# Optimization experiments

Hardware: AMD Instinct MI355X
Metric: run time of the kernel (lower is better)

## Reference

```python
import jax, jax.numpy as jnp
import numpy as np


def setup_inputs() -> dict:
    key = jax.random.key(0)
    k0, k1, k2, k3 = jax.random.split(key, 4)
    B, N, D, C, F = 8192, 784, 64, 10, 2  # batch, input_dim, bond_dim, num_classes, feature_dim
    x = jax.random.uniform(k0, (B, N), dtype=jnp.float32)  # pixel values in [0,1]
    core0 = jax.random.normal(k1, (F, 1, D), dtype=jnp.float32) * 0.1
    base = jnp.broadcast_to(jnp.eye(D, dtype=jnp.float32), (N - 2, F, D, D))
    cores_mid = base + jax.random.normal(k2, (N - 2, F, D, D), dtype=jnp.float32) * 0.01
    core_last = jax.random.normal(k3, (F, D, C), dtype=jnp.float32) * 0.1
    return {"x": x, "core0": core0, "cores_mid": cores_mid, "core_last": core_last}


def reference(x, core0, cores_mid, core_last):
    EPS = 1e-8
    factor = jnp.float32(np.pi / 2.0)
    # FeatureMap: [B, N] -> [B, N, 2] with (cos, sin)
    feats = jnp.stack([jnp.cos(factor * x), jnp.sin(factor * x)], axis=-1)
    # First site: M = v0 @ A0.squeeze(1)  -> [B, D]
    M = jnp.einsum('bf,fd->bd', feats[:, 0, :], core0[:, 0, :])
    # Sequential left->right contraction over middle sites with per-step L2 normalization
    v_mid = jnp.moveaxis(feats[:, 1:-1, :], 1, 0)  # [N-2, B, 2]

    def step(M, inp):
        v, A = inp  # v: [B, 2], A: [2, D, D]
        Mn = jnp.einsum('bi,bf,fij->bj', M, v, A)
        Mn = Mn / (jnp.linalg.norm(Mn, axis=1, keepdims=True) + EPS)
        return Mn, None

    M, _ = jax.lax.scan(step, M, (v_mid, cores_mid))
    # Last site: logits[b,c] = sum_i M[b,i] * (v_N[b,f] A_N[f,i,c])
    logits = jnp.einsum('bi,bf,fic->bc', M, feats[:, -1, :], core_last)
    return logits
```

## Files before the change

kernel.cpp:

```cpp
#include <hip/hip_runtime.h>

typedef __attribute__((ext_vector_type(8))) short s16x8;
typedef __attribute__((ext_vector_type(4))) float f32x4;
typedef __attribute__((ext_vector_type(4))) int i32x4;

#define NMID 782
#define PI_2 1.5707963267948966f
#define EG_STEP_BYTES 16384
#define EG_ELEMS ((size_t)NMID * 8192)
#define SLAB_B 2304
#define DBUF_B 4608

__device__ __forceinline__ int cvt_pk_bf16(float a, float b) {
  int r;
  asm("v_cvt_pk_bf16_f32 %0, %1, %2" : "=v"(r) : "v"(a), "v"(b));
  return r;
}

__device__ __forceinline__ f32x4 mfma_bf16(i32x4 a, i32x4 b, f32x4 c) {
  return __builtin_amdgcn_mfma_f32_16x16x32_bf16(
      __builtin_bit_cast(s16x8, a), __builtin_bit_cast(s16x8, b), c, 0, 0, 0);
}

__device__ __forceinline__ unsigned short bf16_rne(float v) {
  unsigned u = __float_as_uint(v);
  return (unsigned short)((u + 0x7FFFu + ((u >> 16) & 1)) >> 16);
}

__global__ __launch_bounds__(256) void prep_eg(const float* __restrict__ cm,
                                               unsigned short* __restrict__ eg) {
  const int n = blockIdx.x;
  const float* src = cm + (size_t)n * 8192;
  unsigned short* dst = eg + (size_t)n * 8192;
#pragma unroll
  for (int it = 0; it < 4; ++it) {
    int row = it * 256 + threadIdx.x;
    int q = row >> 6, l = row & 63;
    int t = q >> 2, cc = q & 3;
    int f = cc >> 1, c2 = cc & 1, h = l >> 4;
    int j = 16 * t + (l & 15);
    unsigned short v8[8];
#pragma unroll
    for (int e = 0; e < 8; ++e) {
      int i = 32 * c2 + 16 * (e >> 2) + 4 * h + (e & 3);
      float val = src[(f * 64 + i) * 64 + j] - (i == j ? 1.0f : 0.0f);
      v8[e] = bf16_rne(val);
    }
    *(uint4*)(dst + (size_t)row * 8) = *(const uint4*)v8;
  }
}

#define STEP2G(nc, CUR, NXT, C0, S0, C1, S1)                                \
  {                                                                         \
    int np = (nc) + 3;                                                      \
    if (np >= NMID) np = NMID - 1;                                          \
    const char* pnxt = base + (size_t)np * EG_STEP_BYTES;                   \
    _Pragma("unroll") for (int q = 0; q < 4; ++q)                           \
        NXT[q] = *(const i32x4*)(pnxt + q * 1024);                          \
    f32x4 z = {0.f, 0.f, 0.f, 0.f};                                         \
    __builtin_amdgcn_s_setprio(1);                                          \
    f32x4 aA0 = mfma_bf16(CUR[0], B0g0, z);                                 \
    aA0 = mfma_bf16(CUR[1], B1g0, aA0);                                     \
    f32x4 aB0 = mfma_bf16(CUR[2], B0g0, z);                                 \
    aB0 = mfma_bf16(CUR[3], B1g0, aB0);                                     \
    f32x4 aA1 = mfma_bf16(CUR[0], B0g1, z);                                 \
    aA1 = mfma_bf16(CUR[1], B1g1, aA1);                                     \
    f32x4 aB1 = mfma_bf16(CUR[2], B0g1, z);                                 \
    aB1 = mfma_bf16(CUR[3], B1g1, aB1);                                     \
    __builtin_amdgcn_s_setprio(0);                                          \
    char* wb = xlds + (((nc) + 1) & 1) * DBUF_B + bl * 144 + h * 32 +       \
               wv * 8;                                                      \
    float cps0 = (C0) + (S0);                                               \
    f32x4 mn0;                                                              \
    _Pragma("unroll") for (int r = 0; r < 4; ++r)                           \
        mn0[r] = cps0 * own0[r] + (C0)*aA0[r] + (S0)*aB0[r];                \
    own0 = mn0;                                                             \
    int2 w0;                                                                \
    w0.x = cvt_pk_bf16(mn0[0], mn0[1]);                                     \
    w0.y = cvt_pk_bf16(mn0[2], mn0[3]);                                     \
    *(int2*)(wb) = w0;                                                      \
    float cps1 = (C1) + (S1);                                               \
    f32x4 mn1;                                                              \
    _Pragma("unroll") for (int r = 0; r < 4; ++r)                           \
        mn1[r] = cps1 * own1[r] + (C1)*aA1[r] + (S1)*aB1[r];                \
    own1 = mn1;                                                             \
    int2 w1;                                                                \
    w1.x = cvt_pk_bf16(mn1[0], mn1[1]);                                     \
    w1.y = cvt_pk_bf16(mn1[2], mn1[3]);                                     \
    *(int2*)(wb + SLAB_B) = w1;                                             \
    asm volatile("s_waitcnt lgkmcnt(0)" ::: "memory");                      \
    __builtin_amdgcn_s_barrier();                                           \
    __builtin_amdgcn_sched_barrier(0);                                      \
    {                                                                       \
      const char* rb =                                                      \
          xlds + (((nc) + 1) & 1) * DBUF_B + bl * 144 + h * 32;             \
      B0g0 = *(const i32x4*)(rb);                                           \
      B1g0 = *(const i32x4*)(rb + 16);                                      \
      B0g1 = *(const i32x4*)(rb + SLAB_B);                                  \
      B1g1 = *(const i32x4*)(rb + SLAB_B + 16);                             \
    }                                                                       \
  }

__global__ __launch_bounds__(256, 1) void mps_main(
    const float* __restrict__ x, const float* __restrict__ core0,
    const float* __restrict__ core_last, const unsigned short* __restrict__ eg,
    float* __restrict__ out) {
  __shared__ alignas(16) char xlds[2 * DBUF_B];
  const int lane = threadIdx.x & 63;
  const int wv = threadIdx.x >> 6;
  const int bl = lane & 15;
  const int h = lane >> 4;
  const int b0 = blockIdx.x * 32 + bl;
  const int b1 = b0 + 16;
  const float* xr0 = x + (size_t)b0 * 784;
  const float* xr1 = x + (size_t)b1 * 784;
  const char* base = (const char*)eg + (size_t)wv * 4096 + (size_t)lane * 16;

  f32x4 own0, own1;
  i32x4 B0g0, B1g0, B0g1, B1g1;
  {
    float s, c;
    __sincosf(PI_2 * xr0[0], &s, &c);
    float fm[16];
#pragma unroll
    for (int t = 0; t < 4; ++t)
#pragma unroll
      for (int r = 0; r < 4; ++r) {
        int j = 16 * t + 4 * h + r;
        fm[t * 4 + r] = c * core0[j] + s * core0[64 + j];
      }
#pragma unroll
    for (int r = 0; r < 4; ++r) own0[r] = fm[wv * 4 + r];
#pragma unroll
    for (int p = 0; p < 4; ++p) {
      B0g0[p] = cvt_pk_bf16(fm[2 * p], fm[2 * p + 1]);
      B1g0[p] = cvt_pk_bf16(fm[8 + 2 * p], fm[8 + 2 * p + 1]);
    }
  }
  {
    float s, c;
    __sincosf(PI_2 * xr1[0], &s, &c);
    float fm[16];
#pragma unroll
    for (int t = 0; t < 4; ++t)
#pragma unroll
      for (int r = 0; r < 4; ++r) {
        int j = 16 * t + 4 * h + r;
        fm[t * 4 + r] = c * core0[j] + s * core0[64 + j];
      }
#pragma unroll
    for (int r = 0; r < 4; ++r) own1[r] = fm[wv * 4 + r];
#pragma unroll
    for (int p = 0; p < 4; ++p) {
      B0g1[p] = cvt_pk_bf16(fm[2 * p], fm[2 * p + 1]);
      B1g1[p] = cvt_pk_bf16(fm[8 + 2 * p], fm[8 + 2 * p + 1]);
    }
  }

  i32x4 frA[4], frB[4], frC[4], frD[4];
#pragma unroll
  for (int q = 0; q < 4; ++q)
    frA[q] = *(const i32x4*)(base + 0 * EG_STEP_BYTES + q * 1024);
#pragma unroll
  for (int q = 0; q < 4; ++q)
    frB[q] = *(const i32x4*)(base + 1 * EG_STEP_BYTES + q * 1024);
#pragma unroll
  for (int q = 0; q < 4; ++q)
    frC[q] = *(const i32x4*)(base + 2 * EG_STEP_BYTES + q * 1024);

  float xq0[16], xqn0[16], xq1[16], xqn1[16];
  *(f32x4*)&xq0[0] = *(const f32x4*)(xr0 + 0);
  *(f32x4*)&xq0[4] = *(const f32x4*)(xr0 + 4);
  *(f32x4*)&xq0[8] = *(const f32x4*)(xr0 + 8);
  *(f32x4*)&xq0[12] = *(const f32x4*)(xr0 + 12);
  *(f32x4*)&xq1[0] = *(const f32x4*)(xr1 + 0);
  *(f32x4*)&xq1[4] = *(const f32x4*)(xr1 + 4);
  *(f32x4*)&xq1[8] = *(const f32x4*)(xr1 + 8);
  *(f32x4*)&xq1[12] = *(const f32x4*)(xr1 + 12);

  for (int g = 0; g < 65; ++g) {
    if (g < 64) {
      const float* xp0 = xr0 + 12 * (g + 1);
      *(f32x4*)&xqn0[0] = *(const f32x4*)(xp0 + 0);
      *(f32x4*)&xqn0[4] = *(const f32x4*)(xp0 + 4);
      *(f32x4*)&xqn0[8] = *(const f32x4*)(xp0 + 8);
      *(f32x4*)&xqn0[12] = *(const f32x4*)(xp0 + 12);
      const float* xp1 = xr1 + 12 * (g + 1);
      *(f32x4*)&xqn1[0] = *(const f32x4*)(xp1 + 0);
      *(f32x4*)&xqn1[4] = *(const f32x4*)(xp1 + 4);
      *(f32x4*)&xqn1[8] = *(const f32x4*)(xp1 + 8);
      *(f32x4*)&xqn1[12] = *(const f32x4*)(xp1 + 12);
    } else {
      *(f32x4*)&xqn0[0] = *(const f32x4*)(xr0 + 780);
      *(f32x4*)&xqn1[0] = *(const f32x4*)(xr1 + 780);
    }

    float cg0[12], sg0[12], cg1[12], sg1[12];
#pragma unroll
    for (int k = 0; k < 12; ++k) {
      __sincosf(PI_2 * xq0[1 + k], &sg0[k], &cg0[k]);
      __sincosf(PI_2 * xq1[1 + k], &sg1[k], &cg1[k]);
    }

    if (g % 5 == 0) {
      float ss0 = 0.f, ss1 = 0.f;
#pragma unroll
      for (int p = 0; p < 4; ++p) {
        unsigned u0 = (unsigned)B0g0[p], u1 = (unsigned)B1g0[p];
        float a0 = __uint_as_float(u0 << 16);
        float a1 = __uint_as_float(u0 & 0xFFFF0000u);
        float d0 = __uint_as_float(u1 << 16);
        float d1 = __uint_as_float(u1 & 0xFFFF0000u);
        ss0 += a0 * a0 + a1 * a1 + d0 * d0 + d1 * d1;
        unsigned v0 = (unsigned)B0g1[p], v1 = (unsigned)B1g1[p];
        float e0 = __uint_as_float(v0 << 16);
        float e1 = __uint_as_float(v0 & 0xFFFF0000u);
        float f0 = __uint_as_float(v1 << 16);
        float f1 = __uint_as_float(v1 & 0xFFFF0000u);
        ss1 += e0 * e0 + e1 * e1 + f0 * f0 + f1 * f1;
      }
      ss0 += __shfl_xor(ss0, 16);
      ss0 += __shfl_xor(ss0, 32);
      ss1 += __shfl_xor(ss1, 16);
      ss1 += __shfl_xor(ss1, 32);
      float inv0 = rsqrtf(ss0), inv1 = rsqrtf(ss1);
      cg0[0] *= inv0;
      sg0[0] *= inv0;
      cg1[0] *= inv1;
      sg1[0] *= inv1;
    }

    int n0 = 12 * g;
    STEP2G(n0 + 0, frA, frD, cg0[0], sg0[0], cg1[0], sg1[0]);
    STEP2G(n0 + 1, frB, frA, cg0[1], sg0[1], cg1[1], sg1[1]);
    STEP2G(n0 + 2, frC, frB, cg0[2], sg0[2], cg1[2], sg1[2]);
    STEP2G(n0 + 3, frD, frC, cg0[3], sg0[3], cg1[3], sg1[3]);
    STEP2G(n0 + 4, frA, frD, cg0[4], sg0[4], cg1[4], sg1[4]);
    STEP2G(n0 + 5, frB, frA, cg0[5], sg0[5], cg1[5], sg1[5]);
    STEP2G(n0 + 6, frC, frB, cg0[6], sg0[6], cg1[6], sg1[6]);
    STEP2G(n0 + 7, frD, frC, cg0[7], sg0[7], cg1[7], sg1[7]);
    STEP2G(n0 + 8, frA, frD, cg0[8], sg0[8], cg1[8], sg1[8]);
    STEP2G(n0 + 9, frB, frA, cg0[9], sg0[9], cg1[9], sg1[9]);
    STEP2G(n0 + 10, frC, frB, cg0[10], sg0[10], cg1[10], sg1[10]);
    STEP2G(n0 + 11, frD, frC, cg0[11], sg0[11], cg1[11], sg1[11]);

#pragma unroll
    for (int i = 0; i < 16; ++i) {
      xq0[i] = xqn0[i];
      xq1[i] = xqn1[i];
    }
  }

  {
    float c00, s00, c01, s01, c10, s10, c11, s11;
    __sincosf(PI_2 * xq0[1], &s00, &c00);
    __sincosf(PI_2 * xq0[2], &s01, &c01);
    __sincosf(PI_2 * xq1[1], &s10, &c10);
    __sincosf(PI_2 * xq1[2], &s11, &c11);
    STEP2G(780, frA, frD, c00, s00, c10, s10);
    STEP2G(781, frB, frA, c01, s01, c11, s11);
  }

  asm volatile("s_waitcnt lgkmcnt(0)" ::: "memory");
  __builtin_amdgcn_s_barrier();
  *(f32x4*)(xlds + wv * 1152 + lane * 16) = own0;
  *(f32x4*)(xlds + DBUF_B + wv * 1152 + lane * 16) = own1;
  asm volatile("s_waitcnt lgkmcnt(0)" ::: "memory");
  __builtin_amdgcn_s_barrier();
  __builtin_amdgcn_sched_barrier(0);

#pragma unroll
  for (int grp = 0; grp < 2; ++grp) {
    float fm[16];
#pragma unroll
    for (int t = 0; t < 4; ++t) {
      f32x4 v =
          *(const f32x4*)(xlds + grp * DBUF_B + t * 1152 + lane * 16);
#pragma unroll
      for (int r = 0; r < 4; ++r) fm[t * 4 + r] = v[r];
    }
    float ss = 0.f;
#pragma unroll
    for (int i = 0; i < 16; ++i) ss += fm[i] * fm[i];
    ss += __shfl_xor(ss, 16);
    ss += __shfl_xor(ss, 32);
    float inv = 1.0f / (sqrtf(ss) + 1e-8f);
#pragma unroll
    for (int i = 0; i < 16; ++i) fm[i] *= inv;

    float xv = grp == 0 ? xq0[3] : xq1[3];
    float s, c;
    __sincosf(PI_2 * xv, &s, &c);
    float part[10];
#pragma unroll
    for (int cc = 0; cc < 10; ++cc) part[cc] = 0.f;
#pragma unroll
    for (int t = 0; t < 4; ++t)
#pragma unroll
      for (int r = 0; r < 4; ++r) {
        int i = 16 * t + 4 * h + r;
        float mv = fm[t * 4 + r];
#pragma unroll
        for (int cc = 0; cc < 10; ++cc)
          part[cc] +=
              mv * (c * core_last[i * 10 + cc] + s * core_last[640 + i * 10 + cc]);
      }
#pragma unroll
    for (int cc = 0; cc < 10; ++cc) {
      part[cc] += __shfl_xor(part[cc], 16);
      part[cc] += __shfl_xor(part[cc], 32);
    }
    if (wv == 0 && h == 0) {
      int brow = grp == 0 ? b0 : b1;
#pragma unroll
      for (int cc = 0; cc < 10; ++cc) out[brow * 10 + cc] = part[cc];
    }
  }
}

__global__ __launch_bounds__(64) void mps_slow(const float* __restrict__ x,
                                               const float* __restrict__ core0,
                                               const float* __restrict__ cm,
                                               const float* __restrict__ cl,
                                               float* __restrict__ out) {
  int b = blockIdx.x * 64 + threadIdx.x;
  float m[64], mn[64];
  float s, c;
  __sincosf(PI_2 * x[(size_t)b * 784], &s, &c);
  for (int d = 0; d < 64; ++d) m[d] = c * core0[d] + s * core0[64 + d];
  for (int n = 0; n < NMID; ++n) {
    __sincosf(PI_2 * x[(size_t)b * 784 + n + 1], &s, &c);
    const float* A0 = cm + (size_t)n * 8192;
    const float* A1 = A0 + 4096;
    for (int j = 0; j < 64; ++j) mn[j] = 0.f;
    for (int i = 0; i < 64; ++i) {
      float w0 = c * m[i], w1 = s * m[i];
      for (int j = 0; j < 64; ++j) mn[j] += w0 * A0[i * 64 + j] + w1 * A1[i * 64 + j];
    }
    float ssn = 0.f;
    for (int j = 0; j < 64; ++j) ssn += mn[j] * mn[j];
    float inv = 1.f / (sqrtf(ssn) + 1e-8f);
    for (int j = 0; j < 64; ++j) m[j] = mn[j] * inv;
  }
  __sincosf(PI_2 * x[(size_t)b * 784 + 783], &s, &c);
  for (int cc = 0; cc < 10; ++cc) {
    float acc = 0.f;
    for (int i = 0; i < 64; ++i)
      acc += m[i] * (c * cl[i * 10 + cc] + s * cl[640 + i * 10 + cc]);
    out[b * 10 + cc] = acc;
  }
}

extern "C" void kernel_launch(void* const* d_in, const int* in_sizes, int n_in,
                              void* d_out, int out_size, void* d_ws, size_t ws_size,
                              hipStream_t stream) {
  const float* x = (const float*)d_in[0];
  const float* core0 = (const float*)d_in[1];
  const float* cm = (const float*)d_in[2];
  const float* cl = (const float*)d_in[3];
  float* out = (float*)d_out;
  size_t need = EG_ELEMS * sizeof(unsigned short);
  if (ws_size >= need) {
    unsigned short* eg = (unsigned short*)d_ws;
    prep_eg<<<NMID, 256, 0, stream>>>(cm, eg);
    mps_main<<<256, 256, 0, stream>>>(x, core0, cl, eg, out);
  } else {
    mps_slow<<<8192 / 64, 64, 0, stream>>>(x, core0, cm, cl, out);
  }
}
```

Before: 279.4 us.

## Cut register pressure to allow two blocks per CU with inline sincos

```diff
diff --git a/kernel.cpp b/kernel.cpp
--- a/kernel.cpp
+++ b/kernel.cpp
@@ -8,8 +8,8 @@
 #define PI_2 1.5707963267948966f
 #define EG_STEP_BYTES 16384
 #define EG_ELEMS ((size_t)NMID * 8192)
-#define SLAB_B 2304
-#define DBUF_B 4608
+#define XCH_CH 3072
+#define XCH_PAR 6144
 
 __device__ __forceinline__ int cvt_pk_bf16(float a, float b) {
   int r;
@@ -50,13 +50,20 @@
   }
 }
 
-#define STEP2G(nc, CUR, NXT, C0, S0, C1, S1)                                \
+#define STEP2G(nc, CUR, NXT, X0v, X1v, RS0, RS1)                            \
   {                                                                         \
     int np = (nc) + 3;                                                      \
     if (np >= NMID) np = NMID - 1;                                          \
     const char* pnxt = base + (size_t)np * EG_STEP_BYTES;                   \
     _Pragma("unroll") for (int q = 0; q < 4; ++q)                           \
         NXT[q] = *(const i32x4*)(pnxt + q * 1024);                          \
+    float c0, s0, c1, s1;                                                   \
+    __sincosf(PI_2 * (X0v), &s0, &c0);                                      \
+    __sincosf(PI_2 * (X1v), &s1, &c1);                                      \
+    c0 *= (RS0);                                                            \
+    s0 *= (RS0);                                                            \
+    c1 *= (RS1);                                                            \
+    s1 *= (RS1);                                                            \
     f32x4 z = {0.f, 0.f, 0.f, 0.f};                                         \
     __builtin_amdgcn_s_setprio(1);                                          \
     f32x4 aA0 = mfma_bf16(CUR[0], B0g0, z);                                 \
@@ -68,44 +75,44 @@
     f32x4 aB1 = mfma_bf16(CUR[2], B0g1, z);                                 \
     aB1 = mfma_bf16(CUR[3], B1g1, aB1);                                     \
     __builtin_amdgcn_s_setprio(0);                                          \
-    char* wb = xlds + (((nc) + 1) & 1) * DBUF_B + bl * 144 + h * 32 +       \
+    char* wb = xlds + (((nc) + 1) & 1) * XCH_PAR + h * 768 + bl * 48 +      \
                wv * 8;                                                      \
-    float cps0 = (C0) + (S0);                                               \
+    float cps0 = c0 + s0;                                                   \
     f32x4 mn0;                                                              \
     _Pragma("unroll") for (int r = 0; r < 4; ++r)                           \
-        mn0[r] = cps0 * own0[r] + (C0)*aA0[r] + (S0)*aB0[r];                \
+        mn0[r] = cps0 * own0[r] + c0 * aA0[r] + s0 * aB0[r];                \
     own0 = mn0;                                                             \
     int2 w0;                                                                \
     w0.x = cvt_pk_bf16(mn0[0], mn0[1]);                                     \
     w0.y = cvt_pk_bf16(mn0[2], mn0[3]);                                     \
     *(int2*)(wb) = w0;                                                      \
-    float cps1 = (C1) + (S1);                                               \
+    float cps1 = c1 + s1;                                                   \
     f32x4 mn1;                                                              \
     _Pragma("unroll") for (int r = 0; r < 4; ++r)                           \
-        mn1[r] = cps1 * own1[r] + (C1)*aA1[r] + (S1)*aB1[r];                \
+        mn1[r] = cps1 * own1[r] + c1 * aA1[r] + s1 * aB1[r];                \
     own1 = mn1;                                                             \
     int2 w1;                                                                \
     w1.x = cvt_pk_bf16(mn1[0], mn1[1]);                                     \
     w1.y = cvt_pk_bf16(mn1[2], mn1[3]);                                     \
-    *(int2*)(wb + SLAB_B) = w1;                                             \
+    *(int2*)(wb + XCH_CH) = w1;                                             \
     asm volatile("s_waitcnt lgkmcnt(0)" ::: "memory");                      \
     __builtin_amdgcn_s_barrier();                                           \
     __builtin_amdgcn_sched_barrier(0);                                      \
     {                                                                       \
       const char* rb =                                                      \
-          xlds + (((nc) + 1) & 1) * DBUF_B + bl * 144 + h * 32;             \
+          xlds + (((nc) + 1) & 1) * XCH_PAR + h * 768 + bl * 48;            \
       B0g0 = *(const i32x4*)(rb);                                           \
       B1g0 = *(const i32x4*)(rb + 16);                                      \
-      B0g1 = *(const i32x4*)(rb + SLAB_B);                                  \
-      B1g1 = *(const i32x4*)(rb + SLAB_B + 16);                             \
+      B0g1 = *(const i32x4*)(rb + XCH_CH);                                  \
+      B1g1 = *(const i32x4*)(rb + XCH_CH + 16);                             \
     }                                                                       \
   }
 
-__global__ __launch_bounds__(256, 1) void mps_main(
+__global__ __launch_bounds__(256, 2) void mps_main(
     const float* __restrict__ x, const float* __restrict__ core0,
     const float* __restrict__ core_last, const unsigned short* __restrict__ eg,
     float* __restrict__ out) {
-  __shared__ alignas(16) char xlds[2 * DBUF_B];
+  __shared__ alignas(16) char xlds[2 * XCH_PAR];
   const int lane = threadIdx.x & 63;
   const int wv = threadIdx.x >> 6;
   const int bl = lane & 15;
@@ -168,41 +175,38 @@
   for (int q = 0; q < 4; ++q)
     frC[q] = *(const i32x4*)(base + 2 * EG_STEP_BYTES + q * 1024);
 
-  float xq0[16], xqn0[16], xq1[16], xqn1[16];
+  float xq0[12], xq1[12];
+  f32x4 xfA0, xfB0, xfA1, xfB1;
   *(f32x4*)&xq0[0] = *(const f32x4*)(xr0 + 0);
   *(f32x4*)&xq0[4] = *(const f32x4*)(xr0 + 4);
   *(f32x4*)&xq0[8] = *(const f32x4*)(xr0 + 8);
-  *(f32x4*)&xq0[12] = *(const f32x4*)(xr0 + 12);
   *(f32x4*)&xq1[0] = *(const f32x4*)(xr1 + 0);
   *(f32x4*)&xq1[4] = *(const f32x4*)(xr1 + 4);
   *(f32x4*)&xq1[8] = *(const f32x4*)(xr1 + 8);
-  *(f32x4*)&xq1[12] = *(const f32x4*)(xr1 + 12);
-
-  for (int g = 0; g < 65; ++g) {
-    if (g < 64) {
-      const float* xp0 = xr0 + 12 * (g + 1);
-      *(f32x4*)&xqn0[0] = *(const f32x4*)(xp0 + 0);
-      *(f32x4*)&xqn0[4] = *(const f32x4*)(xp0 + 4);
-      *(f32x4*)&xqn0[8] = *(const f32x4*)(xp0 + 8);
-      *(f32x4*)&xqn0[12] = *(const f32x4*)(xp0 + 12);
-      const float* xp1 = xr1 + 12 * (g + 1);
-      *(f32x4*)&xqn1[0] = *(const f32x4*)(xp1 + 0);
-      *(f32x4*)&xqn1[4] = *(const f32x4*)(xp1 + 4);
-      *(f32x4*)&xqn1[8] = *(const f32x4*)(xp1 + 8);
-      *(f32x4*)&xqn1[12] = *(const f32x4*)(xp1 + 12);
-    } else {
-      *(f32x4*)&xqn0[0] = *(const f32x4*)(xr0 + 780);
-      *(f32x4*)&xqn1[0] = *(const f32x4*)(xr1 + 780);
-    }
-
-    float cg0[12], sg0[12], cg1[12], sg1[12];
-#pragma unroll
-    for (int k = 0; k < 12; ++k) {
-      __sincosf(PI_2 * xq0[1 + k], &sg0[k], &cg0[k]);
-      __sincosf(PI_2 * xq1[1 + k], &sg1[k], &cg1[k]);
-    }
-
-    if (g % 5 == 0) {
+
+  for (int g = 0; g < 97; ++g) {
+    if (g > 0) {
+#pragma unroll
+      for (int i = 0; i < 4; ++i) {
+        xq0[i] = xq0[8 + i];
+        xq1[i] = xq1[8 + i];
+      }
+      *(f32x4*)&xq0[4] = xfA0;
+      *(f32x4*)&xq0[8] = xfB0;
+      *(f32x4*)&xq1[4] = xfA1;
+      *(f32x4*)&xq1[8] = xfB1;
+    }
+    {
+      int xo = (g < 96) ? 8 * g + 12 : 780;
+      int xo2 = (g < 96) ? 8 * g + 16 : 780;
+      xfA0 = *(const f32x4*)(xr0 + xo);
+      xfB0 = *(const f32x4*)(xr0 + xo2);
+      xfA1 = *(const f32x4*)(xr1 + xo);
+      xfB1 = *(const f32x4*)(xr1 + xo2);
+    }
+
+    float rs0 = 1.0f, rs1 = 1.0f;
+    if ((g & 7) == 0) {
       float ss0 = 0.f, ss1 = 0.f;
 #pragma unroll
       for (int p = 0; p < 4; ++p) {
@@ -223,48 +227,41 @@
       ss0 += __shfl_xor(ss0, 32);
       ss1 += __shfl_xor(ss1, 16);
       ss1 += __shfl_xor(ss1, 32);
-      float inv0 = rsqrtf(ss0), inv1 = rsqrtf(ss1);
-      cg0[0] *= inv0;
-      sg0[0] *= inv0;
-      cg1[0] *= inv1;
-      sg1[0] *= inv1;
-    }
-
-    int n0 = 12 * g;
-    STEP2G(n0 + 0, frA, frD, cg0[0], sg0[0], cg1[0], sg1[0]);
-    STEP2G(n0 + 1, frB, frA, cg0[1], sg0[1], cg1[1], sg1[1]);
-    STEP2G(n0 + 2, frC, frB, cg0[2], sg0[2], cg1[2], sg1[2]);
-    STEP2G(n0 + 3, frD, frC, cg0[3], sg0[3], cg1[3], sg1[3]);
-    STEP2G(n0 + 4, frA, frD, cg0[4], sg0[4], cg1[4], sg1[4]);
-    STEP2G(n0 + 5, frB, frA, cg0[5], sg0[5], cg1[5], sg1[5]);
-    STEP2G(n0 + 6, frC, frB, cg0[6], sg0[6], cg1[6], sg1[6]);
-    STEP2G(n0 + 7, frD, frC, cg0[7], sg0[7], cg1[7], sg1[7]);
-    STEP2G(n0 + 8, frA, frD, cg0[8], sg0[8], cg1[8], sg1[8]);
-    STEP2G(n0 + 9, frB, frA, cg0[9], sg0[9], cg1[9], sg1[9]);
-    STEP2G(n0 + 10, frC, frB, cg0[10], sg0[10], cg1[10], sg1[10]);
-    STEP2G(n0 + 11, frD, frC, cg0[11], sg0[11], cg1[11], sg1[11]);
-
-#pragma unroll
-    for (int i = 0; i < 16; ++i) {
-      xq0[i] = xqn0[i];
-      xq1[i] = xqn1[i];
-    }
+      rs0 = rsqrtf(ss0);
+      rs1 = rsqrtf(ss1);
+    }
+
+    int n0 = 8 * g;
+    STEP2G(n0 + 0, frA, frD, xq0[1], xq1[1], rs0, rs1);
+    STEP2G(n0 + 1, frB, frA, xq0[2], xq1[2], 1.0f, 1.0f);
+    STEP2G(n0 + 2, frC, frB, xq0[3], xq1[3], 1.0f, 1.0f);
+    STEP2G(n0 + 3, frD, frC, xq0[4], xq1[4], 1.0f, 1.0f);
+    STEP2G(n0 + 4, frA, frD, xq0[5], xq1[5], 1.0f, 1.0f);
+    STEP2G(n0 + 5, frB, frA, xq0[6], xq1[6], 1.0f, 1.0f);
+    STEP2G(n0 + 6, frC, frB, xq0[7], xq1[7], 1.0f, 1.0f);
+    STEP2G(n0 + 7, frD, frC, xq0[8], xq1[8], 1.0f, 1.0f);
   }
 
   {
-    float c00, s00, c01, s01, c10, s10, c11, s11;
-    __sincosf(PI_2 * xq0[1], &s00, &c00);
-    __sincosf(PI_2 * xq0[2], &s01, &c01);
-    __sincosf(PI_2 * xq1[1], &s10, &c10);
-    __sincosf(PI_2 * xq1[2], &s11, &c11);
-    STEP2G(780, frA, frD, c00, s00, c10, s10);
-    STEP2G(781, frB, frA, c01, s01, c11, s11);
+#pragma unroll
+    for (int i = 0; i < 4; ++i) {
+      xq0[i] = xq0[8 + i];
+      xq1[i] = xq1[8 + i];
+    }
+    *(f32x4*)&xq0[4] = xfA0;
+    *(f32x4*)&xq1[4] = xfA1;
+    STEP2G(776, frA, frD, xq0[1], xq1[1], 1.0f, 1.0f);
+    STEP2G(777, frB, frA, xq0[2], xq1[2], 1.0f, 1.0f);
+    STEP2G(778, frC, frB, xq0[3], xq1[3], 1.0f, 1.0f);
+    STEP2G(779, frD, frC, xq0[4], xq1[4], 1.0f, 1.0f);
+    STEP2G(780, frA, frD, xq0[5], xq1[5], 1.0f, 1.0f);
+    STEP2G(781, frB, frA, xq0[6], xq1[6], 1.0f, 1.0f);
   }
 
   asm volatile("s_waitcnt lgkmcnt(0)" ::: "memory");
   __builtin_amdgcn_s_barrier();
   *(f32x4*)(xlds + wv * 1152 + lane * 16) = own0;
-  *(f32x4*)(xlds + DBUF_B + wv * 1152 + lane * 16) = own1;
+  *(f32x4*)(xlds + 4608 + wv * 1152 + lane * 16) = own1;
   asm volatile("s_waitcnt lgkmcnt(0)" ::: "memory");
   __builtin_amdgcn_s_barrier();
   __builtin_amdgcn_sched_barrier(0);
@@ -274,8 +271,7 @@
     float fm[16];
 #pragma unroll
     for (int t = 0; t < 4; ++t) {
-      f32x4 v =
-          *(const f32x4*)(xlds + grp * DBUF_B + t * 1152 + lane * 16);
+      f32x4 v = *(const f32x4*)(xlds + grp * 4608 + t * 1152 + lane * 16);
 #pragma unroll
       for (int r = 0; r < 4; ++r) fm[t * 4 + r] = v[r];
     }
@@ -288,7 +284,7 @@
 #pragma unroll
     for (int i = 0; i < 16; ++i) fm[i] *= inv;
 
-    float xv = grp == 0 ? xq0[3] : xq1[3];
+    float xv = grp == 0 ? xq0[7] : xq1[7];
     float s, c;
     __sincosf(PI_2 * xv, &s, &c);
     float part[10];
```

Result: faster. 245.9 us (median of 2 runs) (-12.0%).
